# Kernel tuning notes

Measured on AMD Instinct MI355X. Metric: run time of the kernel, lower is better.

The kernel has to match this reference:

```python
import jax, jax.numpy as jnp
import numpy as np

HIDDEN = 1024
STATE = 16
BATCH = 4
SEQ = 2048


def setup_inputs() -> dict:
    key = jax.random.key(0)
    k0, k1, k2, k3 = jax.random.split(key, 4)
    x = jax.random.normal(k0, (BATCH, SEQ, HIDDEN), jnp.float32)
    # nn.Linear(hidden, 2*state + hidden, bias=False): weight shape (out, in)
    Wx = jax.random.normal(k1, (2 * STATE + HIDDEN, HIDDEN), jnp.float32) / np.sqrt(HIDDEN)
    A_log = jax.random.normal(k2, (STATE,), jnp.float32)
    D = jnp.ones((HIDDEN,), jnp.float32)
    Wout = jax.random.normal(k3, (HIDDEN, HIDDEN), jnp.float32) / np.sqrt(HIDDEN)
    return {"x": x, "Wx": Wx, "A_log": A_log, "D": D, "Wout": Wout}


def reference(x, Wx, A_log, D, Wout):
    B, L, H = x.shape
    N = A_log.shape[0]
    xp = x @ Wx.T                                   # (B,L,2N+H)
    Bm = xp[..., :N]                                # (B,L,N)
    Cm = xp[..., N:2 * N]                           # (B,L,N)
    delta = jax.nn.softplus(xp[..., 2 * N:])        # (B,L,H)
    A = -jnp.exp(A_log)                             # (N,)

    def step(h, inp):
        dt, bt, ct, xt = inp                        # (B,H),(B,N),(B,N),(B,H)
        dA = jnp.exp(dt[:, None, :] * A[None, :, None])        # (B,N,H)
        h = dA * h + (dt[:, None, :] * bt[:, :, None]) * xt[:, None, :]
        y = jnp.einsum('bnh,bn->bh', h, ct) + D * xt
        return h, y

    h0 = jnp.zeros((B, N, H), x.dtype)
    xs = (jnp.swapaxes(delta, 0, 1), jnp.swapaxes(Bm, 0, 1),
          jnp.swapaxes(Cm, 0, 1), jnp.swapaxes(x, 0, 1))
    _, ys = jax.lax.scan(step, h0, xs)              # ys: (L,B,H)
    y = jnp.swapaxes(ys, 0, 1)                      # (B,L,H)
    return y @ Wout.T
```

## Files before the change

### kernel.cpp

```cpp
#include <hip/hip_runtime.h>

#define HDIM 1024
#define LSEQ 2048
#define NBATCH 4
#define NS 16
#define BL (NBATCH * LSEQ)
#define KDIM 1024
#define NX 1056
#define NXPAD 1152
#define NCHUNK 64
#define CLEN 32

typedef unsigned short u16;
typedef short short8 __attribute__((ext_vector_type(8)));
typedef float f32x4 __attribute__((ext_vector_type(4)));
typedef u16 u16x8 __attribute__((ext_vector_type(8)));
typedef u16 u16x2 __attribute__((ext_vector_type(2)));

__device__ __forceinline__ u16 f2bf(float f) {
  union { float f; unsigned u; } v; v.f = f;
  unsigned r = v.u + 0x7fffu + ((v.u >> 16) & 1u);
  return (u16)(r >> 16);
}
__device__ __forceinline__ float bf2f(u16 b) {
  union { unsigned u; float f; } v; v.u = ((unsigned)b) << 16; return v.f;
}
__device__ __forceinline__ u16 f2h(float f) {
  union { _Float16 h; u16 u; } v; v.h = (_Float16)f; return v.u;
}
__device__ __forceinline__ float h2f(u16 h) {
  union { u16 u; _Float16 h; } v; v.u = h; return (float)v.h;
}

__device__ __forceinline__ void ld16(const void* g, void* l) {
  __builtin_amdgcn_global_load_lds(
      (const __attribute__((address_space(1))) unsigned int*)g,
      (__attribute__((address_space(3))) unsigned int*)l, 16, 0, 0);
}

__device__ __forceinline__ void rbar() {
  asm volatile("" ::: "memory");
  __builtin_amdgcn_s_barrier();
  asm volatile("" ::: "memory");
}

__global__ __launch_bounds__(256) void cvt_all_kernel(const float* __restrict__ x,
                                                      const float* __restrict__ Wx,
                                                      const float* __restrict__ Wout,
                                                      u16* __restrict__ x_bf,
                                                      u16* __restrict__ wx_bf,
                                                      u16* __restrict__ wo_bf) {
  const int blk = blockIdx.x;
  const float* in;
  u16* out;
  int i;
  bool zero = false;
  if (blk < 4096) {
    i = (blk * 256 + threadIdx.x) * 8;
    in = x; out = x_bf;
  } else if (blk < 4672) {
    i = ((blk - 4096) * 256 + threadIdx.x) * 8;
    in = Wx; out = wx_bf;
    zero = (i >> 10) >= NX;
  } else {
    i = ((blk - 4672) * 256 + threadIdx.x) * 8;
    in = Wout; out = wo_bf;
  }
  u16x8 r;
  if (!zero) {
    float4 a = *(const float4*)(in + i);
    float4 b = *(const float4*)(in + i + 4);
    r[0] = f2bf(a.x); r[1] = f2bf(a.y); r[2] = f2bf(a.z); r[3] = f2bf(a.w);
    r[4] = f2bf(b.x); r[5] = f2bf(b.y); r[6] = f2bf(b.z); r[7] = f2bf(b.w);
  } else {
#pragma unroll
    for (int t = 0; t < 8; ++t) r[t] = 0;
  }
  *(u16x8*)(out + i) = r;
}

template <int EPI>
__global__ __launch_bounds__(256) void gemm_bt(const u16* __restrict__ A,
                                               const u16* __restrict__ B,
                                               float* __restrict__ C,
                                               float* __restrict__ Bmo,
                                               float* __restrict__ Cmo,
                                               u16* __restrict__ Dlo,
                                               int N) {
  __shared__ __align__(16) u16 S[2][32 * 512];
  const int tid = threadIdx.x, lane = tid & 63, w = tid >> 6;
  const int m0 = blockIdx.x * 128, n0 = blockIdx.y * 128;
  const int lr = lane & 15, lq = lane >> 4;
  const int wr = w >> 1, wc = w & 1;
  f32x4 acc[4][4] = {};

  const u16* ga[4]; const u16* gb[4];
  int loA[4], loB[4];
#pragma unroll
  for (int c = 0; c < 4; ++c) {
    const int ca = w * 4 + c;
    const int row = ((ca >> 1) << 4) + lr;
    const int col = ((ca & 1) << 5) + (lq << 3);
    ga[c] = A + (size_t)(m0 + row) * KDIM + col;
    gb[c] = B + (size_t)(n0 + row) * KDIM + col;
    loA[c] = ca * 512;
    loB[c] = (16 + ca) * 512;
  }

  auto stage = [&](int buf) {
    u16* base = &S[buf][0];
#pragma unroll
    for (int c = 0; c < 4; ++c) {
      ld16(ga[c], base + loA[c]);
      ld16(gb[c], base + loB[c]);
      ga[c] += 64; gb[c] += 64;
    }
  };

  auto compute = [&](int buf) {
    const u16* base = &S[buf][0];
#pragma unroll
    for (int kh = 0; kh < 2; ++kh) {
      short8 af[4], bfr[4];
#pragma unroll
      for (int i = 0; i < 4; ++i)
        af[i] = *(const short8*)(base + ((wr * 4 + i) * 2 + kh) * 512 + lane * 8);
#pragma unroll
      for (int j = 0; j < 4; ++j)
        bfr[j] = *(const short8*)(base + (16 + (wc * 4 + j) * 2 + kh) * 512 + lane * 8);
#pragma unroll
      for (int i = 0; i < 4; ++i)
#pragma unroll
        for (int j = 0; j < 4; ++j)
          acc[i][j] = __builtin_amdgcn_mfma_f32_16x16x32_bf16(af[i], bfr[j], acc[i][j], 0, 0, 0);
    }
  };

  stage(0);
  stage(1);
  asm volatile("s_waitcnt vmcnt(8)" ::: "memory");
  rbar();
  int cur = 0;
  for (int kt = 0; kt < KDIM / 64 - 2; ++kt) {
    compute(cur);
    rbar();
    stage(cur);
    asm volatile("s_waitcnt vmcnt(8)" ::: "memory");
    rbar();
    cur ^= 1;
  }
  compute(cur);
  asm volatile("s_waitcnt vmcnt(0)" ::: "memory");
  rbar();
  compute(cur ^ 1);

#pragma unroll
  for (int i = 0; i < 4; ++i) {
    const int gr0 = m0 + wr * 64 + i * 16 + lq * 4;
#pragma unroll
    for (int j = 0; j < 4; ++j) {
      const int gc = n0 + wc * 64 + j * 16 + lr;
      if (EPI == 0) {
        float* p = C + (size_t)gr0 * N + gc;
#pragma unroll
        for (int r = 0; r < 4; ++r) p[(size_t)r * N] = acc[i][j][r];
      } else {
        const int nt = gc >> 4;
        if (nt == 0) {
#pragma unroll
          for (int r = 0; r < 4; ++r) Bmo[(gr0 + r) * NS + lr] = acc[i][j][r];
        } else if (nt == 1) {
#pragma unroll
          for (int r = 0; r < 4; ++r) Cmo[(gr0 + r) * NS + lr] = acc[i][j][r];
        } else if (nt < 66) {
#pragma unroll
          for (int r = 0; r < 4; ++r) {
            float v = acc[i][j][r];
            float sp = fmaxf(v, 0.f) + __logf(1.f + __expf(-fabsf(v)));
            Dlo[(size_t)(gr0 + r) * HDIM + (gc - 2 * NS)] = f2h(sp);
          }
        }
      }
    }
  }
}

template <int PHASE>
__global__ __launch_bounds__(256) void scan_phase(
    const u16* __restrict__ dlth, const u16* __restrict__ xb,
    const float* __restrict__ Bm, const float* __restrict__ Cm,
    const float* __restrict__ A_log, const float* __restrict__ Dvec,
    float* __restrict__ hbuf,
    float* __restrict__ dts_out,
    u16* __restrict__ yout) {
  __shared__ __align__(16) float sbt[CLEN][16];
  __shared__ __align__(16) float sct[CLEN][16];
  const int tid = threadIdx.x, lane = tid & 63, w = tid >> 6;
  const int b = blockIdx.x >> 6, c = blockIdx.x & 63;
  const int h = (blockIdx.y << 9) + tid * 2;
  const size_t l0 = (size_t)b * LSEQ + (size_t)c * CLEN;

  if (w == 0) {
#pragma unroll
    for (int i = 0; i < 2; ++i)
      ld16(Bm + l0 * NS + i * 256 + lane * 4, (void*)(&sbt[0][0] + i * 256));
  } else if (w == 1 && PHASE == 3) {
#pragma unroll
    for (int i = 0; i < 2; ++i)
      ld16(Cm + l0 * NS + i * 256 + lane * 4, (void*)(&sct[0][0] + i * 256));
  }

  const u16* pd = dlth + l0 * HDIM + h;
  const u16* px = xb + l0 * HDIM + h;

  float Ae[16], hs[16][2];
#pragma unroll
  for (int n = 0; n < 16; ++n) Ae[n] = -expf(A_log[n]) * 1.44269504088896f;
  if (PHASE == 3 && c > 0) {
    const float* hp = hbuf + ((size_t)b * NCHUNK + (c - 1)) * NS * HDIM + h;
#pragma unroll
    for (int n = 0; n < 16; ++n) {
      const float2 t = *(const float2*)(hp + (size_t)n * HDIM);
      hs[n][0] = t.x; hs[n][1] = t.y;
    }
  } else {
#pragma unroll
    for (int n = 0; n < 16; ++n) { hs[n][0] = 0.f; hs[n][1] = 0.f; }
  }
  float Dh0 = 0.f, Dh1 = 0.f;
  if (PHASE == 3) { Dh0 = Dvec[h]; Dh1 = Dvec[h + 1]; }
  float dts0 = 0.f, dts1 = 0.f;

  u16x2 d0[8], x0[8], d1[8], x1[8];
  auto loadb = [&](int ks, u16x2* dd, u16x2* xx) {
#pragma unroll
    for (int j = 0; j < 8; ++j) {
      dd[j] = *(const u16x2*)(pd + (size_t)(ks * 8 + j) * HDIM);
      xx[j] = *(const u16x2*)(px + (size_t)(ks * 8 + j) * HDIM);
    }
  };
  auto compute = [&](int ks, const u16x2* dd, const u16x2* xx) {
#pragma unroll
    for (int s = 0; s < 8; ++s) {
      const int l = ks * 8 + s;
      const float dt0 = h2f(dd[s][0]), dt1 = h2f(dd[s][1]);
      const float xt0 = bf2f(xx[s][0]), xt1 = bf2f(xx[s][1]);
      const float dx0 = dt0 * xt0, dx1 = dt1 * xt1;
      if (PHASE == 1) { dts0 += dt0; dts1 += dt1; }
      float y0 = Dh0 * xt0, y1 = Dh1 * xt1;
      const f32x4* btp = (const f32x4*)&sbt[l][0];
      const f32x4* ctp = (const f32x4*)&sct[l][0];
#pragma unroll
      for (int q = 0; q < 4; ++q) {
        const f32x4 b4 = btp[q];
        f32x4 c4;
        if (PHASE == 3) c4 = ctp[q];
#pragma unroll
        for (int r = 0; r < 4; ++r) {
          const int n = q * 4 + r;
          const float dA0 = __builtin_amdgcn_exp2f(dt0 * Ae[n]);
          const float dA1 = __builtin_amdgcn_exp2f(dt1 * Ae[n]);
          hs[n][0] = fmaf(dA0, hs[n][0], b4[r] * dx0);
          hs[n][1] = fmaf(dA1, hs[n][1], b4[r] * dx1);
          if (PHASE == 3) {
            y0 = fmaf(hs[n][0], c4[r], y0);
            y1 = fmaf(hs[n][1], c4[r], y1);
          }
        }
      }
      if (PHASE == 3) {
        u16x2 yo; yo[0] = f2bf(y0); yo[1] = f2bf(y1);
        *(u16x2*)(yout + (l0 + l) * HDIM + h) = yo;
      }
    }
  };

  loadb(0, d0, x0);
  loadb(1, d1, x1);
  __syncthreads();
  compute(0, d0, x0); loadb(2, d0, x0);
  compute(1, d1, x1); loadb(3, d1, x1);
  compute(2, d0, x0);
  compute(3, d1, x1);

  if (PHASE == 1) {
    float* hp = hbuf + ((size_t)b * NCHUNK + c) * NS * HDIM + h;
#pragma unroll
    for (int n = 0; n < 16; ++n)
      *(float2*)(hp + (size_t)n * HDIM) = float2{hs[n][0], hs[n][1]};
    *(float2*)(dts_out + ((size_t)b * NCHUNK + c) * HDIM + h) = float2{dts0, dts1};
  }
}

__global__ __launch_bounds__(256) void scan_combine(
    float* __restrict__ hbuf, const float* __restrict__ dts,
    const float* __restrict__ A_log) {
  const int id = blockIdx.x * 256 + threadIdx.x;
  const int h = id & (HDIM - 1);
  const int n = (id >> 10) & (NS - 1);
  const int b = id >> 14;
  const float Ae = -expf(A_log[n]) * 1.44269504088896f;
  const size_t hstride = (size_t)NS * HDIM;
  float* hp = hbuf + ((size_t)b * NCHUNK * NS + n) * HDIM + h;
  const float* dp = dts + (size_t)b * NCHUNK * HDIM + h;
  float hs = 0.f;
  float nh = hp[0];
  float nd = dp[0];
  for (int c = 1; c < NCHUNK; ++c) {
    const float curh = nh, curd = nd;
    if (c < NCHUNK - 1) {
      nh = hp[(size_t)c * hstride];
      nd = dp[(size_t)c * HDIM];
    }
    hs = fmaf(__builtin_amdgcn_exp2f(Ae * curd), hs, curh);
    hp[(size_t)(c - 1) * hstride] = hs;
  }
}

extern "C" void kernel_launch(void* const* d_in, const int* in_sizes, int n_in,
                              void* d_out, int out_size, void* d_ws, size_t ws_size,
                              hipStream_t stream) {
  (void)in_sizes; (void)n_in; (void)out_size; (void)ws_size;
  const float* x     = (const float*)d_in[0];
  const float* Wx    = (const float*)d_in[1];
  const float* A_log = (const float*)d_in[2];
  const float* Dv    = (const float*)d_in[3];
  const float* Wout  = (const float*)d_in[4];
  float* out = (float*)d_out;

  char* ws = (char*)d_ws;
  u16*   x_bf  = (u16*)(ws);
  u16*   wx_bf = (u16*)(ws + 16777216);
  u16*   wo_bf = (u16*)(ws + 19136512);
  u16*   dlth  = (u16*)(ws + 21233664);
  float* hbuf  = (float*)(ws + 38010880);
  float* Bm    = (float*)(ws + 54788096);
  float* Cm    = (float*)(ws + 55312384);
  u16*   y_bf  = (u16*)(ws + 55836672);
  float* dts   = (float*)wx_bf;

  cvt_all_kernel<<<5184, 256, 0, stream>>>(x, Wx, Wout, x_bf, wx_bf, wo_bf);

  dim3 g1(BL / 128, NXPAD / 128);
  gemm_bt<1><<<g1, 256, 0, stream>>>(x_bf, wx_bf, nullptr, Bm, Cm, dlth, NXPAD);

  dim3 gs(NBATCH * NCHUNK, HDIM / 512);
  scan_phase<1><<<gs, 256, 0, stream>>>(dlth, x_bf, Bm, Cm, A_log, Dv, hbuf, dts, nullptr);
  scan_combine<<<256, 256, 0, stream>>>(hbuf, dts, A_log);
  scan_phase<3><<<gs, 256, 0, stream>>>(dlth, x_bf, Bm, Cm, A_log, Dv, hbuf, dts, y_bf);

  dim3 g3(BL / 128, HDIM / 128);
  gemm_bt<0><<<g3, 256, 0, stream>>>(y_bf, wo_bf, out, nullptr, nullptr, nullptr, HDIM);
}
```

Measured before the change: 242.4 us.

## Give each wavefront private LDS staging to remove block barriers in GEMM

Restructures the GEMM main loop so that each wavefront loads its own A and B fragments (64 rows each, K-step 32) into a private LDS region, replacing the block-wide s_barrier calls with per-wave waitcnt and scheduling barriers. This removes inter-wave synchronisation stalls, at the cost of losing data sharing between waves. Each A and B tile is now fetched twice from global memory, and each iteration does half the K work with the same number of waitcnts, so global and L2 traffic per block rises.

```diff
diff --git a/kernel.cpp b/kernel.cpp
--- a/kernel.cpp
+++ b/kernel.cpp
@@ -38,11 +38,7 @@
       (__attribute__((address_space(3))) unsigned int*)l, 16, 0, 0);
 }
 
-__device__ __forceinline__ void rbar() {
-  asm volatile("" ::: "memory");
-  __builtin_amdgcn_s_barrier();
-  asm volatile("" ::: "memory");
-}
+__device__ __forceinline__ void cfence() { asm volatile("" ::: "memory"); }
 
 __global__ __launch_bounds__(256) void cvt_all_kernel(const float* __restrict__ x,
                                                       const float* __restrict__ Wx,
@@ -87,71 +83,64 @@
                                                float* __restrict__ Cmo,
                                                u16* __restrict__ Dlo,
                                                int N) {
-  __shared__ __align__(16) u16 S[2][32 * 512];
+  __shared__ __align__(16) u16 S[2][4][8 * 512];
   const int tid = threadIdx.x, lane = tid & 63, w = tid >> 6;
   const int m0 = blockIdx.x * 128, n0 = blockIdx.y * 128;
   const int lr = lane & 15, lq = lane >> 4;
   const int wr = w >> 1, wc = w & 1;
   f32x4 acc[4][4] = {};
 
-  const u16* ga[4]; const u16* gb[4];
-  int loA[4], loB[4];
-#pragma unroll
-  for (int c = 0; c < 4; ++c) {
-    const int ca = w * 4 + c;
-    const int row = ((ca >> 1) << 4) + lr;
-    const int col = ((ca & 1) << 5) + (lq << 3);
-    ga[c] = A + (size_t)(m0 + row) * KDIM + col;
-    gb[c] = B + (size_t)(n0 + row) * KDIM + col;
-    loA[c] = ca * 512;
-    loB[c] = (16 + ca) * 512;
+  const u16* gp[8];
+#pragma unroll
+  for (int c = 0; c < 8; ++c) {
+    if (c < 4) {
+      gp[c] = A + (size_t)(m0 + wr * 64 + c * 16 + lr) * KDIM + (lq << 3);
+    } else {
+      gp[c] = B + (size_t)(n0 + wc * 64 + (c - 4) * 16 + lr) * KDIM + (lq << 3);
+    }
   }
 
   auto stage = [&](int buf) {
-    u16* base = &S[buf][0];
-#pragma unroll
-    for (int c = 0; c < 4; ++c) {
-      ld16(ga[c], base + loA[c]);
-      ld16(gb[c], base + loB[c]);
-      ga[c] += 64; gb[c] += 64;
+    u16* base = &S[buf][w][0];
+#pragma unroll
+    for (int c = 0; c < 8; ++c) {
+      ld16(gp[c], base + c * 512);
+      gp[c] += 32;
     }
   };
 
   auto compute = [&](int buf) {
-    const u16* base = &S[buf][0];
-#pragma unroll
-    for (int kh = 0; kh < 2; ++kh) {
-      short8 af[4], bfr[4];
-#pragma unroll
-      for (int i = 0; i < 4; ++i)
-        af[i] = *(const short8*)(base + ((wr * 4 + i) * 2 + kh) * 512 + lane * 8);
+    const u16* base = &S[buf][w][0];
+    short8 af[4], bfr[4];
+#pragma unroll
+    for (int i = 0; i < 4; ++i)
+      af[i] = *(const short8*)(base + i * 512 + lane * 8);
+#pragma unroll
+    for (int j = 0; j < 4; ++j)
+      bfr[j] = *(const short8*)(base + (4 + j) * 512 + lane * 8);
+#pragma unroll
+    for (int i = 0; i < 4; ++i)
 #pragma unroll
       for (int j = 0; j < 4; ++j)
-        bfr[j] = *(const short8*)(base + (16 + (wc * 4 + j) * 2 + kh) * 512 + lane * 8);
-#pragma unroll
-      for (int i = 0; i < 4; ++i)
-#pragma unroll
-        for (int j = 0; j < 4; ++j)
-          acc[i][j] = __builtin_amdgcn_mfma_f32_16x16x32_bf16(af[i], bfr[j], acc[i][j], 0, 0, 0);
-    }
+        acc[i][j] = __builtin_amdgcn_mfma_f32_16x16x32_bf16(af[i], bfr[j], acc[i][j], 0, 0, 0);
   };
 
   stage(0);
   stage(1);
   asm volatile("s_waitcnt vmcnt(8)" ::: "memory");
-  rbar();
+  __builtin_amdgcn_sched_barrier(0);
   int cur = 0;
-  for (int kt = 0; kt < KDIM / 64 - 2; ++kt) {
+  for (int kt = 0; kt < KDIM / 32 - 2; ++kt) {
     compute(cur);
-    rbar();
+    cfence();
     stage(cur);
     asm volatile("s_waitcnt vmcnt(8)" ::: "memory");
-    rbar();
+    __builtin_amdgcn_sched_barrier(0);
     cur ^= 1;
   }
   compute(cur);
   asm volatile("s_waitcnt vmcnt(0)" ::: "memory");
-  rbar();
+  __builtin_amdgcn_sched_barrier(0);
   compute(cur ^ 1);
 
 #pragma unroll
```

Result: slower. 308.7 us (+27.4%).
